# Optimization experiments

Hardware: AMD Instinct MI355X
Metric: run time of the kernel (lower is better)

The kernel has to match this reference:

```python
import jax, jax.numpy as jnp
import numpy as np

H, W = 512, 512
G = 8192
ALPHA_THRESH = 1.0 / 255.0        # meta_f32[0]
TRANS_THRESH = 1.0e-4             # meta_f32[1]
ALPHA_CAP = 0.99                  # meta_f32[6]
BG = jnp.zeros((3,), dtype=jnp.float32)  # config.background


def setup_inputs() -> dict:
    key = jax.random.key(0)
    ks = jax.random.split(key, 7)
    mx = jax.random.uniform(ks[0], (G,), minval=0.0, maxval=float(W))
    my = jax.random.uniform(ks[1], (G,), minval=0.0, maxval=float(H))
    means2d = jnp.stack([mx, my], axis=-1)
    # Build valid conics (inverse 2x2 covariances) from random rotation + scales
    theta = jax.random.uniform(ks[2], (G,), minval=0.0, maxval=2.0 * np.pi)
    s = jax.random.uniform(ks[3], (G, 2), minval=2.0, maxval=12.0)  # px stddevs
    ct, st = jnp.cos(theta), jnp.sin(theta)
    v1, v2 = s[:, 0] ** 2, s[:, 1] ** 2
    ca = ct * ct * v1 + st * st * v2
    cb = ct * st * (v1 - v2)
    cc = st * st * v1 + ct * ct * v2
    det = ca * cc - cb * cb
    conics = jnp.stack([cc / det, -cb / det, ca / det], axis=-1)  # [G,3] = (a,b,c)
    colors = jax.random.uniform(ks[4], (G, 3))
    opacities = jax.random.uniform(ks[5], (G,))
    depths = jax.random.uniform(ks[6], (G,), minval=0.1, maxval=100.0)
    return {"means2d": means2d, "conics": conics, "colors": colors,
            "opacities": opacities, "depths": depths}


def reference(means2d, conics, colors, opacities, depths):
    # Stable front-to-back depth sort (mirrors perm = argsort(depths, stable))
    perm = jnp.argsort(depths, stable=True)
    m = means2d[perm]
    cn = conics[perm]
    col = colors[perm]
    op = opacities[perm]
    a, b, c = cn[:, 0], cn[:, 1], cn[:, 2]
    px = jnp.arange(W, dtype=means2d.dtype) + 0.5  # pixel centers

    def row(y):
        py = y.astype(means2d.dtype) + 0.5
        dx = px[:, None] - m[None, :, 0]          # [W,G]
        dy = py - m[:, 1]                          # [G]
        sigma = 0.5 * (a * dx * dx + c * dy * dy) + b * dx * dy  # [W,G]
        alpha = jnp.minimum(ALPHA_CAP, op * jnp.exp(-sigma))
        alpha = jnp.where((sigma < 0) | (alpha < ALPHA_THRESH), 0.0, alpha)
        # exclusive cumulative transmittance along depth order
        Tprev = jnp.cumprod(1.0 - alpha, axis=-1)
        Tprev = jnp.concatenate([jnp.ones((W, 1), alpha.dtype), Tprev[:, :-1]], axis=-1)
        # early-termination: splats seen after T drops below threshold contribute 0
        wgt = alpha * Tprev * (Tprev >= TRANS_THRESH)  # [W,G]
        rgb = wgt @ col                                 # [W,3]
        t_rem = 1.0 - wgt.sum(axis=-1)                  # remaining transmittance
        return rgb + t_rem[:, None] * BG

    return jax.lax.map(row, jnp.arange(H))  # [H,W,3]
```

## Files before the change

### kernel.cpp

```cpp
#include <hip/hip_runtime.h>

#define G 8192
#define IMG_W 512
#define IMG_H 512
#define TILE 16
#define NTX (IMG_W / TILE)
#define NTY (IMG_H / TILE)
#define BLK 256
#define BLKT 128
#define CAP 1024
#define ALPHA_THRESH (1.0f/255.0f)
#define ALPHA_CAP 0.99f
#define TRANS_THRESH 1e-4f

__global__ __launch_bounds__(BLK)
void range_kernel(const float* __restrict__ means2d,
                  const float* __restrict__ conics,
                  const float* __restrict__ colors,
                  const float* __restrict__ opac,
                  unsigned int* __restrict__ ranges,
                  float* __restrict__ tbl)
{
    int g = blockIdx.x * BLK + threadIdx.x;
    if (g >= G) return;
    float op = opac[g];
    float a  = conics[3*g], b = conics[3*g+1], c = conics[3*g+2];
    float mx = means2d[2*g], my = means2d[2*g+1];
    float cr = colors[3*g], cg = colors[3*g+1], cb = colors[3*g+2];

    float4* t4 = (float4*)(tbl + (g << 4));
    t4[0] = make_float4(mx, my, 0.5f * a, b);
    t4[1] = make_float4(0.5f * c, op, cr, cg);
    t4[2] = make_float4(cb, 0.0f, 0.0f, 0.0f);
    if (g == 0) {
        float4* z = (float4*)(tbl + (G << 4));
        z[0] = z[1] = z[2] = make_float4(0.0f, 0.0f, 0.0f, 0.0f);
    }

    unsigned int packed = 0xFFu;
    if (op * 255.0f >= 1.0f) {
        float smax = __logf(op * 255.0f);
        float det = fmaxf(a * c - b * b, 1e-12f);
        float rx = sqrtf(fmaxf(2.0f * smax * c / det, 0.0f)) * 1.0001f + 0.01f;
        float ry = sqrtf(fmaxf(2.0f * smax * a / det, 0.0f)) * 1.0001f + 0.01f;
        int txmin = (int)ceilf ((mx - rx - 15.5f) * 0.0625f);
        int txmax = (int)floorf((mx + rx -  0.5f) * 0.0625f);
        int tymin = (int)ceilf ((my - ry - 15.5f) * 0.0625f);
        int tymax = (int)floorf((my + ry -  0.5f) * 0.0625f);
        if (!(txmax < 0 || txmin > NTX-1 || tymax < 0 || tymin > NTY-1 ||
              txmin > txmax || tymin > tymax)) {
            txmin = max(txmin, 0); txmax = min(txmax, NTX-1);
            tymin = max(tymin, 0); tymax = min(tymax, NTY-1);
            packed = (unsigned)txmin | ((unsigned)txmax << 8)
                   | ((unsigned)tymin << 16) | ((unsigned)tymax << 24);
        }
    }
    ranges[g] = packed;
}

__device__ __forceinline__ int hitp(unsigned p, unsigned btx, unsigned bty)
{
    return (btx >= (p & 0xffu)) & (btx <= ((p >> 8) & 0xffu)) &
           (bty >= ((p >> 16) & 0xffu)) & (bty <= (p >> 24));
}

__global__ __launch_bounds__(BLKT)
void tile_kernel(const unsigned int* __restrict__ ranges,
                 const float* __restrict__ depths,
                 const float* __restrict__ tbl,
                 float*       __restrict__ out)
{
    __shared__ __align__(16) unsigned short slist[CAP + 4];
    __shared__ __align__(16) unsigned int fkeys[CAP + 4];
    __shared__ int woff[2];

    const int t = threadIdx.x;
    const int lane = t & 63, w = t >> 6;
    const unsigned btx = blockIdx.x, bty = blockIdx.y;

    const uint4* r4 = (const uint4*)ranges;
    const int wbase = w * (G / 2);
    uint4 rv[16];
    #pragma unroll
    for (int i = 0; i < 16; ++i)
        rv[i] = r4[(wbase >> 2) + i * 64 + lane];

    int cnt = 0;
    #pragma unroll
    for (int i = 0; i < 16; ++i)
        cnt += hitp(rv[i].x, btx, bty) + hitp(rv[i].y, btx, bty)
             + hitp(rv[i].z, btx, bty) + hitp(rv[i].w, btx, bty);
    #pragma unroll
    for (int d = 1; d < 64; d <<= 1) cnt += __shfl_xor(cnt, d);
    if (lane == 0) woff[w] = cnt;
    __syncthreads();

    int offs = (w == 1) ? woff[0] : 0;
    const int N = min(woff[0] + woff[1], CAP);

    const unsigned long long lt = (1ull << lane) - 1ull;
    #pragma unroll
    for (int i = 0; i < 16; ++i) {
        int gbase = wbase + i * 256 + lane * 4;
        int h0 = hitp(rv[i].x, btx, bty), h1 = hitp(rv[i].y, btx, bty);
        int h2 = hitp(rv[i].z, btx, bty), h3 = hitp(rv[i].w, btx, bty);
        unsigned long long m0 = __ballot(h0), m1 = __ballot(h1);
        unsigned long long m2 = __ballot(h2), m3 = __ballot(h3);
        int pos = offs + __popcll(m0 & lt) + __popcll(m1 & lt)
                       + __popcll(m2 & lt) + __popcll(m3 & lt);
        if (h0) { if (pos < CAP) slist[pos] = (unsigned short)(gbase    ); pos++; }
        if (h1) { if (pos < CAP) slist[pos] = (unsigned short)(gbase + 1); pos++; }
        if (h2) { if (pos < CAP) slist[pos] = (unsigned short)(gbase + 2); pos++; }
        if (h3) { if (pos < CAP) slist[pos] = (unsigned short)(gbase + 3); pos++; }
        offs += __popcll(m0) + __popcll(m1) + __popcll(m2) + __popcll(m3);
    }
    __syncthreads();

    unsigned short myidx[8]; unsigned int mykey[8]; int myr[8];
    #pragma unroll
    for (int m = 0; m < 8; ++m) {
        int i = t + m * BLKT;
        if (i < N) {
            unsigned idx = slist[i];
            unsigned k = __float_as_uint(depths[idx]);
            myidx[m] = (unsigned short)idx; mykey[m] = k; fkeys[i] = k;
        }
    }
    if (t < 4) fkeys[N + t] = 0xFFFFFFFFu;
    __syncthreads();

    const uint4* fk4 = (const uint4*)fkeys;
    const int nj4 = (N + 3) >> 2;
    #pragma unroll
    for (int m = 0; m < 8; ++m) {
        int i = t + m * BLKT;
        if (i < N) {
            unsigned ke = mykey[m]; int r = 0;
            for (int j4 = 0; j4 < nj4; ++j4) {
                uint4 kv = fk4[j4]; int j = j4 << 2;
                r += (int)((kv.x < ke) | ((kv.x == ke) & (j     < i)));
                r += (int)((kv.y < ke) | ((kv.y == ke) & (j + 1 < i)));
                r += (int)((kv.z < ke) | ((kv.z == ke) & (j + 2 < i)));
                r += (int)((kv.w < ke) | ((kv.w == ke) & (j + 3 < i)));
            }
            myr[m] = r;
        }
    }
    __syncthreads();
    #pragma unroll
    for (int m = 0; m < 8; ++m) {
        int i = t + m * BLKT;
        if (i < N) slist[myr[m]] = myidx[m];
    }
    if (t < 4) slist[N + t] = (unsigned short)G;
    __syncthreads();

    const float px  = (float)(btx * TILE + (lane & 15)) + 0.5f;
    const int   ry  = lane >> 4;
    const float py0 = (float)(bty * TILE + w * 8 + ry * 2) + 0.5f;
    const float py1 = py0 + 1.0f;

    float T0 = 1.0f, T1 = 1.0f;
    float ar0 = 0.f, ag0 = 0.f, ab0 = 0.f;
    float ar1 = 0.f, ag1 = 0.f, ab1 = 0.f;

    for (int base = 0; base < N; base += 4) {
        ushort4 s4 = *(const ushort4*)&slist[base];
        unsigned short sv[4] = { s4.x, s4.y, s4.z, s4.w };
        #pragma unroll
        for (int u = 0; u < 4; ++u) {
            int idx = __builtin_amdgcn_readfirstlane((int)sv[u]);
            const float* r = tbl + (idx << 4);
            float dx = px - r[0];
            float dy0 = py0 - r[1], dy1 = py1 - r[1];
            float sg0 = fmaf(r[2], dx*dx, fmaf(r[4], dy0*dy0, r[3] * (dx*dy0)));
            float sg1 = fmaf(r[2], dx*dx, fmaf(r[4], dy1*dy1, r[3] * (dx*dy1)));
            float al0 = r[5] * __expf(-sg0);
            float al1 = r[5] * __expf(-sg1);
            bool ok0 = (sg0 >= 0.0f) && (al0 >= ALPHA_THRESH);
            bool ok1 = (sg1 >= 0.0f) && (al1 >= ALPHA_THRESH);
            al0 = ok0 ? fminf(al0, ALPHA_CAP) : 0.0f;
            al1 = ok1 ? fminf(al1, ALPHA_CAP) : 0.0f;
            float w0 = al0 * T0, w1 = al1 * T1;
            ar0 = fmaf(w0, r[6], ar0);  ar1 = fmaf(w1, r[6], ar1);
            ag0 = fmaf(w0, r[7], ag0);  ag1 = fmaf(w1, r[7], ag1);
            ab0 = fmaf(w0, r[8], ab0);  ab1 = fmaf(w1, r[8], ab1);
            T0 *= (1.0f - al0);
            T1 *= (1.0f - al1);
        }
        if (__all((T0 < TRANS_THRESH) & (T1 < TRANS_THRESH))) break;
    }

    const int ox = (int)btx * TILE + (lane & 15);
    const int oy = (int)bty * TILE + w * 8 + ry * 2;
    const int o = (oy * IMG_W + ox) * 3;
    out[o]     = ar0;
    out[o + 1] = ag0;
    out[o + 2] = ab0;
    out[o + 3*IMG_W]     = ar1;
    out[o + 3*IMG_W + 1] = ag1;
    out[o + 3*IMG_W + 2] = ab1;
}

extern "C" void kernel_launch(void* const* d_in, const int* in_sizes, int n_in,
                              void* d_out, int out_size, void* d_ws, size_t ws_size,
                              hipStream_t stream)
{
    const float* means2d = (const float*)d_in[0];
    const float* conics  = (const float*)d_in[1];
    const float* colors  = (const float*)d_in[2];
    const float* opac    = (const float*)d_in[3];
    const float* depths  = (const float*)d_in[4];
    float* out = (float*)d_out;
    unsigned int* ranges = (unsigned int*)d_ws;
    float* tbl = (float*)((char*)d_ws + 32 * 1024);

    range_kernel<<<G / BLK, BLK, 0, stream>>>(means2d, conics, colors, opac,
                                              ranges, tbl);
    tile_kernel<<<dim3(NTX, NTY), dim3(BLKT), 0, stream>>>(
        ranges, depths, tbl, out);
}
```

Measured before the change: 98.48 us.

## Double-buffer splat table loads in tile compositing loop with float4 fetches

The per-splat compositing loop now prefetches the next group of four splat records (as float4 vector loads) while computing the current group, ping-ponging between two register sets. Table reads are widened from scalar loads to float4 loads. Sentinel padding of the sorted list and key arrays is enlarged so the lookahead reads stay in bounds. The readfirstlane hint is dropped, so the compiler may emit vector rather than scalar loads, and register pressure rises.

```diff
diff --git a/kernel.cpp b/kernel.cpp
--- a/kernel.cpp
+++ b/kernel.cpp
@@ -64,14 +64,47 @@
            (bty >= ((p >> 16) & 0xffu)) & (bty <= (p >> 24));
 }
 
+#define DECL_GRP(P) \
+    float4 P##0a, P##0b, P##1a, P##1b, P##2a, P##2b, P##3a, P##3b; \
+    float  P##0c, P##1c, P##2c, P##3c;
+
+#define LOAD_GRP(P, s4) { \
+    const float4* b0 = (const float4*)(tbl + ((int)(s4).x << 4)); \
+    const float4* b1 = (const float4*)(tbl + ((int)(s4).y << 4)); \
+    const float4* b2 = (const float4*)(tbl + ((int)(s4).z << 4)); \
+    const float4* b3 = (const float4*)(tbl + ((int)(s4).w << 4)); \
+    P##0a = b0[0]; P##0b = b0[1]; P##0c = ((const float*)b0)[8]; \
+    P##1a = b1[0]; P##1b = b1[1]; P##1c = ((const float*)b1)[8]; \
+    P##2a = b2[0]; P##2b = b2[1]; P##2c = ((const float*)b2)[8]; \
+    P##3a = b3[0]; P##3b = b3[1]; P##3c = ((const float*)b3)[8]; }
+
+#define COMP1(pa, pb, pcb) { \
+    float dx  = px - pa.x; \
+    float dy0 = py0 - pa.y, dy1 = py1 - pa.y; \
+    float dxdx = dx * dx; \
+    float sg0 = fmaf(pa.z, dxdx, fmaf(pb.x, dy0*dy0, pa.w * (dx*dy0))); \
+    float sg1 = fmaf(pa.z, dxdx, fmaf(pb.x, dy1*dy1, pa.w * (dx*dy1))); \
+    float al0 = pb.y * __expf(-sg0); \
+    float al1 = pb.y * __expf(-sg1); \
+    bool ok0 = (sg0 >= 0.0f) && (al0 >= ALPHA_THRESH); \
+    bool ok1 = (sg1 >= 0.0f) && (al1 >= ALPHA_THRESH); \
+    al0 = ok0 ? fminf(al0, ALPHA_CAP) : 0.0f; \
+    al1 = ok1 ? fminf(al1, ALPHA_CAP) : 0.0f; \
+    float w0 = al0 * T0, w1 = al1 * T1; \
+    ar0 = fmaf(w0, pb.z, ar0);  ar1 = fmaf(w1, pb.z, ar1); \
+    ag0 = fmaf(w0, pb.w, ag0);  ag1 = fmaf(w1, pb.w, ag1); \
+    ab0 = fmaf(w0, pcb,  ab0);  ab1 = fmaf(w1, pcb,  ab1); \
+    T0 *= (1.0f - al0); \
+    T1 *= (1.0f - al1); }
+
 __global__ __launch_bounds__(BLKT)
 void tile_kernel(const unsigned int* __restrict__ ranges,
                  const float* __restrict__ depths,
                  const float* __restrict__ tbl,
                  float*       __restrict__ out)
 {
-    __shared__ __align__(16) unsigned short slist[CAP + 4];
-    __shared__ __align__(16) unsigned int fkeys[CAP + 4];
+    __shared__ __align__(16) unsigned short slist[CAP + 16];
+    __shared__ __align__(16) unsigned int fkeys[CAP + 8];
     __shared__ int woff[2];
 
     const int t = threadIdx.x;
@@ -126,7 +159,7 @@
             myidx[m] = (unsigned short)idx; mykey[m] = k; fkeys[i] = k;
         }
     }
-    if (t < 4) fkeys[N + t] = 0xFFFFFFFFu;
+    if (t < 8) fkeys[N + t] = 0xFFFFFFFFu;
     __syncthreads();
 
     const uint4* fk4 = (const uint4*)fkeys;
@@ -152,7 +185,7 @@
         int i = t + m * BLKT;
         if (i < N) slist[myr[m]] = myidx[m];
     }
-    if (t < 4) slist[N + t] = (unsigned short)G;
+    if (t < 16) slist[N + t] = (unsigned short)G;
     __syncthreads();
 
     const float px  = (float)(btx * TILE + (lane & 15)) + 0.5f;
@@ -164,30 +197,29 @@
     float ar0 = 0.f, ag0 = 0.f, ab0 = 0.f;
     float ar1 = 0.f, ag1 = 0.f, ab1 = 0.f;
 
-    for (int base = 0; base < N; base += 4) {
-        ushort4 s4 = *(const ushort4*)&slist[base];
-        unsigned short sv[4] = { s4.x, s4.y, s4.z, s4.w };
-        #pragma unroll
-        for (int u = 0; u < 4; ++u) {
-            int idx = __builtin_amdgcn_readfirstlane((int)sv[u]);
-            const float* r = tbl + (idx << 4);
-            float dx = px - r[0];
-            float dy0 = py0 - r[1], dy1 = py1 - r[1];
-            float sg0 = fmaf(r[2], dx*dx, fmaf(r[4], dy0*dy0, r[3] * (dx*dy0)));
-            float sg1 = fmaf(r[2], dx*dx, fmaf(r[4], dy1*dy1, r[3] * (dx*dy1)));
-            float al0 = r[5] * __expf(-sg0);
-            float al1 = r[5] * __expf(-sg1);
-            bool ok0 = (sg0 >= 0.0f) && (al0 >= ALPHA_THRESH);
-            bool ok1 = (sg1 >= 0.0f) && (al1 >= ALPHA_THRESH);
-            al0 = ok0 ? fminf(al0, ALPHA_CAP) : 0.0f;
-            al1 = ok1 ? fminf(al1, ALPHA_CAP) : 0.0f;
-            float w0 = al0 * T0, w1 = al1 * T1;
-            ar0 = fmaf(w0, r[6], ar0);  ar1 = fmaf(w1, r[6], ar1);
-            ag0 = fmaf(w0, r[7], ag0);  ag1 = fmaf(w1, r[7], ag1);
-            ab0 = fmaf(w0, r[8], ab0);  ab1 = fmaf(w1, r[8], ab1);
-            T0 *= (1.0f - al0);
-            T1 *= (1.0f - al1);
-        }
+    DECL_GRP(A) DECL_GRP(B)
+    ushort4 sB;
+    {
+        ushort4 sA = *(const ushort4*)&slist[0];
+        sB = *(const ushort4*)&slist[4];
+        LOAD_GRP(A, sA)
+    }
+
+    const int nb = (N + 7) & ~7;
+    for (int base = 0; base < nb; base += 8) {
+        ushort4 sA2 = *(const ushort4*)&slist[base + 8];
+        ushort4 sB2 = *(const ushort4*)&slist[base + 12];
+        LOAD_GRP(B, sB)
+        COMP1(A0a, A0b, A0c)
+        COMP1(A1a, A1b, A1c)
+        COMP1(A2a, A2b, A2c)
+        COMP1(A3a, A3b, A3c)
+        LOAD_GRP(A, sA2)
+        COMP1(B0a, B0b, B0c)
+        COMP1(B1a, B1b, B1c)
+        COMP1(B2a, B2b, B2c)
+        COMP1(B3a, B3b, B3c)
+        sB = sB2;
         if (__all((T0 < TRANS_THRESH) & (T1 < TRANS_THRESH))) break;
     }
 
```

After: 97.51 us. About the same (-1.0%).

## Use 16x32 tiles with 256 threads and stage splat params in shared memory

Applied to the files above, without the earlier changes.

Doubles the tile height and uses 256-thread blocks. The per-tile splat list and its rank sort are now built across four wavefronts. During compositing, each batch of up to 256 depth-sorted splat records is loaded cooperatively into shared memory, replacing the per-wavefront scalar global loads, and early termination becomes a per-thread flag combined with a block-wide AND after each batch. The aim is to amortise parameter fetches across more pixels and give each block more threads. The cost is larger per-tile lists, quadratic rank-sort work that grows with list length, fewer blocks, and extra block barriers.

```diff
diff --git a/kernel.cpp b/kernel.cpp
--- a/kernel.cpp
+++ b/kernel.cpp
@@ -3,12 +3,12 @@
 #define G 8192
 #define IMG_W 512
 #define IMG_H 512
-#define TILE 16
-#define NTX (IMG_W / TILE)
-#define NTY (IMG_H / TILE)
+#define TW 16
+#define TH 32
+#define NTX (IMG_W / TW)
+#define NTY (IMG_H / TH)
 #define BLK 256
-#define BLKT 128
-#define CAP 1024
+#define CAP 2048
 #define ALPHA_THRESH (1.0f/255.0f)
 #define ALPHA_CAP 0.99f
 #define TRANS_THRESH 1e-4f
@@ -32,10 +32,6 @@
     t4[0] = make_float4(mx, my, 0.5f * a, b);
     t4[1] = make_float4(0.5f * c, op, cr, cg);
     t4[2] = make_float4(cb, 0.0f, 0.0f, 0.0f);
-    if (g == 0) {
-        float4* z = (float4*)(tbl + (G << 4));
-        z[0] = z[1] = z[2] = make_float4(0.0f, 0.0f, 0.0f, 0.0f);
-    }
 
     unsigned int packed = 0xFFu;
     if (op * 255.0f >= 1.0f) {
@@ -45,8 +41,8 @@
         float ry = sqrtf(fmaxf(2.0f * smax * a / det, 0.0f)) * 1.0001f + 0.01f;
         int txmin = (int)ceilf ((mx - rx - 15.5f) * 0.0625f);
         int txmax = (int)floorf((mx + rx -  0.5f) * 0.0625f);
-        int tymin = (int)ceilf ((my - ry - 15.5f) * 0.0625f);
-        int tymax = (int)floorf((my + ry -  0.5f) * 0.0625f);
+        int tymin = (int)ceilf ((my - ry - 31.5f) * 0.03125f);
+        int tymax = (int)floorf((my + ry -  0.5f) * 0.03125f);
         if (!(txmax < 0 || txmin > NTX-1 || tymax < 0 || tymin > NTY-1 ||
               txmin > txmax || tymin > tymax)) {
             txmin = max(txmin, 0); txmax = min(txmax, NTX-1);
@@ -64,30 +60,33 @@
            (bty >= ((p >> 16) & 0xffu)) & (bty <= (p >> 24));
 }
 
-__global__ __launch_bounds__(BLKT)
+__global__ __launch_bounds__(BLK)
 void tile_kernel(const unsigned int* __restrict__ ranges,
                  const float* __restrict__ depths,
                  const float* __restrict__ tbl,
                  float*       __restrict__ out)
 {
-    __shared__ __align__(16) unsigned short slist[CAP + 4];
-    __shared__ __align__(16) unsigned int fkeys[CAP + 4];
-    __shared__ int woff[2];
+    __shared__ __align__(16) unsigned short slist[CAP];
+    __shared__ __align__(16) unsigned int fkeys[CAP + 8];
+    __shared__ int woff[4];
+    __shared__ float4 sq0[BLK];
+    __shared__ float4 sq1[BLK];
+    __shared__ float  sq2[BLK];
 
     const int t = threadIdx.x;
     const int lane = t & 63, w = t >> 6;
     const unsigned btx = blockIdx.x, bty = blockIdx.y;
 
     const uint4* r4 = (const uint4*)ranges;
-    const int wbase = w * (G / 2);
-    uint4 rv[16];
-    #pragma unroll
-    for (int i = 0; i < 16; ++i)
+    const int wbase = w * (G / 4);
+    uint4 rv[8];
+    #pragma unroll
+    for (int i = 0; i < 8; ++i)
         rv[i] = r4[(wbase >> 2) + i * 64 + lane];
 
     int cnt = 0;
     #pragma unroll
-    for (int i = 0; i < 16; ++i)
+    for (int i = 0; i < 8; ++i)
         cnt += hitp(rv[i].x, btx, bty) + hitp(rv[i].y, btx, bty)
              + hitp(rv[i].z, btx, bty) + hitp(rv[i].w, btx, bty);
     #pragma unroll
@@ -95,12 +94,13 @@
     if (lane == 0) woff[w] = cnt;
     __syncthreads();
 
-    int offs = (w == 1) ? woff[0] : 0;
-    const int N = min(woff[0] + woff[1], CAP);
+    int offs = 0;
+    for (int ww = 0; ww < w; ++ww) offs += woff[ww];
+    const int N = min(woff[0] + woff[1] + woff[2] + woff[3], CAP);
 
     const unsigned long long lt = (1ull << lane) - 1ull;
     #pragma unroll
-    for (int i = 0; i < 16; ++i) {
+    for (int i = 0; i < 8; ++i) {
         int gbase = wbase + i * 256 + lane * 4;
         int h0 = hitp(rv[i].x, btx, bty), h1 = hitp(rv[i].y, btx, bty);
         int h2 = hitp(rv[i].z, btx, bty), h3 = hitp(rv[i].w, btx, bty);
@@ -119,21 +119,21 @@
     unsigned short myidx[8]; unsigned int mykey[8]; int myr[8];
     #pragma unroll
     for (int m = 0; m < 8; ++m) {
-        int i = t + m * BLKT;
+        int i = t + m * BLK;
         if (i < N) {
             unsigned idx = slist[i];
             unsigned k = __float_as_uint(depths[idx]);
             myidx[m] = (unsigned short)idx; mykey[m] = k; fkeys[i] = k;
         }
     }
-    if (t < 4) fkeys[N + t] = 0xFFFFFFFFu;
+    if (t < 8) fkeys[N + t] = 0xFFFFFFFFu;
     __syncthreads();
 
     const uint4* fk4 = (const uint4*)fkeys;
     const int nj4 = (N + 3) >> 2;
     #pragma unroll
     for (int m = 0; m < 8; ++m) {
-        int i = t + m * BLKT;
+        int i = t + m * BLK;
         if (i < N) {
             unsigned ke = mykey[m]; int r = 0;
             for (int j4 = 0; j4 < nj4; ++j4) {
@@ -149,50 +149,69 @@
     __syncthreads();
     #pragma unroll
     for (int m = 0; m < 8; ++m) {
-        int i = t + m * BLKT;
+        int i = t + m * BLK;
         if (i < N) slist[myr[m]] = myidx[m];
     }
-    if (t < 4) slist[N + t] = (unsigned short)G;
-    __syncthreads();
-
-    const float px  = (float)(btx * TILE + (lane & 15)) + 0.5f;
-    const int   ry  = lane >> 4;
-    const float py0 = (float)(bty * TILE + w * 8 + ry * 2) + 0.5f;
+    __syncthreads();
+
+    const float px  = (float)(btx * TW + (t & 15)) + 0.5f;
+    const float py0 = (float)(bty * TH + (t >> 4) * 2) + 0.5f;
     const float py1 = py0 + 1.0f;
 
     float T0 = 1.0f, T1 = 1.0f;
     float ar0 = 0.f, ag0 = 0.f, ab0 = 0.f;
     float ar1 = 0.f, ag1 = 0.f, ab1 = 0.f;
-
-    for (int base = 0; base < N; base += 4) {
-        ushort4 s4 = *(const ushort4*)&slist[base];
-        unsigned short sv[4] = { s4.x, s4.y, s4.z, s4.w };
-        #pragma unroll
-        for (int u = 0; u < 4; ++u) {
-            int idx = __builtin_amdgcn_readfirstlane((int)sv[u]);
-            const float* r = tbl + (idx << 4);
-            float dx = px - r[0];
-            float dy0 = py0 - r[1], dy1 = py1 - r[1];
-            float sg0 = fmaf(r[2], dx*dx, fmaf(r[4], dy0*dy0, r[3] * (dx*dy0)));
-            float sg1 = fmaf(r[2], dx*dx, fmaf(r[4], dy1*dy1, r[3] * (dx*dy1)));
-            float al0 = r[5] * __expf(-sg0);
-            float al1 = r[5] * __expf(-sg1);
-            bool ok0 = (sg0 >= 0.0f) && (al0 >= ALPHA_THRESH);
-            bool ok1 = (sg1 >= 0.0f) && (al1 >= ALPHA_THRESH);
-            al0 = ok0 ? fminf(al0, ALPHA_CAP) : 0.0f;
-            al1 = ok1 ? fminf(al1, ALPHA_CAP) : 0.0f;
-            float w0 = al0 * T0, w1 = al1 * T1;
-            ar0 = fmaf(w0, r[6], ar0);  ar1 = fmaf(w1, r[6], ar1);
-            ag0 = fmaf(w0, r[7], ag0);  ag1 = fmaf(w1, r[7], ag1);
-            ab0 = fmaf(w0, r[8], ab0);  ab1 = fmaf(w1, r[8], ab1);
-            T0 *= (1.0f - al0);
-            T1 *= (1.0f - al1);
-        }
-        if (__all((T0 < TRANS_THRESH) & (T1 < TRANS_THRESH))) break;
-    }
-
-    const int ox = (int)btx * TILE + (lane & 15);
-    const int oy = (int)bty * TILE + w * 8 + ry * 2;
+    bool done = false;
+
+    for (int base = 0; base < N; base += BLK) {
+        int n = min(BLK, N - base);
+        float4 v0 = make_float4(0.f, 0.f, 0.f, 0.f);
+        float4 v1 = make_float4(0.f, 0.f, 0.f, 0.f);
+        float  v2 = 0.f;
+        if (t < n) {
+            int idx = slist[base + t];
+            const float4* b = (const float4*)(tbl + (idx << 4));
+            v0 = b[0]; v1 = b[1]; v2 = ((const float*)b)[8];
+        }
+        sq0[t] = v0; sq1[t] = v1; sq2[t] = v2;
+        __syncthreads();
+
+        if (!done) {
+            int n4 = (n + 3) & ~3;
+            for (int i = 0; i < n4 && !done; i += 4) {
+                #pragma unroll
+                for (int u = 0; u < 4; ++u) {
+                    float4 q0 = sq0[i + u];
+                    float4 q1 = sq1[i + u];
+                    float  bl = sq2[i + u];
+                    float dx  = px  - q0.x;
+                    float dy0 = py0 - q0.y, dy1 = py1 - q0.y;
+                    float dxdx = dx * dx;
+                    float sg0 = fmaf(q0.z, dxdx,
+                                fmaf(q1.x, dy0*dy0, q0.w * (dx*dy0)));
+                    float sg1 = fmaf(q0.z, dxdx,
+                                fmaf(q1.x, dy1*dy1, q0.w * (dx*dy1)));
+                    float al0 = q1.y * __expf(-sg0);
+                    float al1 = q1.y * __expf(-sg1);
+                    bool ok0 = (sg0 >= 0.0f) && (al0 >= ALPHA_THRESH);
+                    bool ok1 = (sg1 >= 0.0f) && (al1 >= ALPHA_THRESH);
+                    al0 = ok0 ? fminf(al0, ALPHA_CAP) : 0.0f;
+                    al1 = ok1 ? fminf(al1, ALPHA_CAP) : 0.0f;
+                    float w0 = al0 * T0, w1 = al1 * T1;
+                    ar0 = fmaf(w0, q1.z, ar0);  ar1 = fmaf(w1, q1.z, ar1);
+                    ag0 = fmaf(w0, q1.w, ag0);  ag1 = fmaf(w1, q1.w, ag1);
+                    ab0 = fmaf(w0, bl,   ab0);  ab1 = fmaf(w1, bl,   ab1);
+                    T0 *= (1.0f - al0);
+                    T1 *= (1.0f - al1);
+                }
+                if ((T0 < TRANS_THRESH) & (T1 < TRANS_THRESH)) done = true;
+            }
+        }
+        if (__syncthreads_and((int)done)) break;
+    }
+
+    const int ox = (int)btx * TW + (t & 15);
+    const int oy = (int)bty * TH + (t >> 4) * 2;
     const int o = (oy * IMG_W + ox) * 3;
     out[o]     = ar0;
     out[o + 1] = ag0;
@@ -217,6 +236,6 @@
 
     range_kernel<<<G / BLK, BLK, 0, stream>>>(means2d, conics, colors, opac,
                                               ranges, tbl);
-    tile_kernel<<<dim3(NTX, NTY), dim3(BLKT), 0, stream>>>(
+    tile_kernel<<<dim3(NTX, NTY), dim3(BLK), 0, stream>>>(
         ranges, depths, tbl, out);
 }
```

Result: faster. 94.10 us (-4.4%).
